# Kernel optimization log

Measured on AMD Instinct MI355X. Metric: run time of the kernel, lower is better.

The kernel has to match this reference:

```python
import jax, jax.numpy as jnp
import numpy as np

B, S, H, D = 8, 2048, 16, 64  # batch, seq, heads, head_dim
DM = H * D                    # d_model = 1024
W = 4                         # compression window / stride


def setup_inputs() -> dict:
    key = jax.random.key(0)
    ks = jax.random.split(key, 6)
    return {
        "pre_q": jax.random.normal(ks[0], (B, S, H, D), dtype=jnp.float32),
        "pre_k": jax.random.normal(ks[1], (B, S, H, D), dtype=jnp.float32),
        "pre_v": jax.random.normal(ks[2], (B, S, H, D), dtype=jnp.float32),
        "k_conv_kernel": jax.random.normal(ks[3], (W, D, D), dtype=jnp.float32) * (1.0 / np.sqrt(W * D)),
        "k_conv_bias": jnp.zeros((D,), dtype=jnp.float32),
        "v_conv_kernel": jax.random.normal(ks[4], (W, D, D), dtype=jnp.float32) * (1.0 / np.sqrt(W * D)),
        "v_conv_bias": jnp.zeros((D,), dtype=jnp.float32),
        "output_weights": jax.random.normal(ks[5], (DM, DM), dtype=jnp.float32) * (1.0 / np.sqrt(DM)),
        "compression_window": W,
    }


def _compress(x, kernel, bias, window):
    # x: [B, H, S, D] -> strided valid conv along seq -> [B, H, Sc, D]
    b, h, s, d = x.shape
    x2 = x.reshape(b * h, s, d)  # NWC
    y = jax.lax.conv_general_dilated(
        x2, kernel, window_strides=(window,), padding="VALID",
        dimension_numbers=("NWC", "WIO", "NWC")) + bias
    return y.reshape(b, h, -1, d)


def reference(pre_q, pre_k, pre_v, k_conv_kernel, k_conv_bias,
              v_conv_kernel, v_conv_bias, output_weights, compression_window):
    b, s, h, d = pre_q.shape
    q = jnp.transpose(pre_q, (0, 2, 1, 3))  # [B,H,S,D]
    k = jnp.transpose(pre_k, (0, 2, 1, 3))
    v = jnp.transpose(pre_v, (0, 2, 1, 3))
    kc = _compress(k, k_conv_kernel, k_conv_bias, compression_window)  # [B,H,Sc,D]
    vc = _compress(v, v_conv_kernel, v_conv_bias, compression_window)
    scale = 1.0 / np.sqrt(d).astype(np.float32)
    scores = jnp.einsum("bhsd,bhtd->bhst", q, kc) * scale  # [B,H,S,Sc]
    attn = jax.nn.softmax(scores, axis=-1)
    out = jnp.einsum("bhst,bhtd->bhsd", attn, vc)  # [B,H,S,D]
    out = jnp.transpose(out, (0, 2, 1, 3)).reshape(b, s, h * d)  # [B,S,DM]
    return out @ output_weights  # [B,S,DM]
```

## Files before the change

kernel.cpp:

```cpp
#include <hip/hip_runtime.h>
#include <hip/hip_bf16.h>
#include <math.h>

#define B_   8
#define S_   2048
#define H_   16
#define D_   64
#define DM_  1024
#define W_   4
#define SC_  512

typedef float f32x4 __attribute__((ext_vector_type(4)));
typedef short bf16x8 __attribute__((ext_vector_type(8)));
typedef short bf16x4 __attribute__((ext_vector_type(4)));

static __device__ inline short f2bf(float f) {
    union { float f; unsigned u; } v; v.f = f;
    unsigned r = v.u + 0x7fffu + ((v.u >> 16) & 1u);
    return (short)(r >> 16);
}

static __device__ inline short bfc(float f) {
    __hip_bfloat16 h = __float2bfloat16(f);
    union { __hip_bfloat16 h; short s; } u; u.h = h; return u.s;
}

static __device__ inline float fexp2(float x) {
    float r; asm("v_exp_f32 %0, %1" : "=v"(r) : "v"(x)); return r;
}

__global__ __launch_bounds__(256) void wtrans_kernel(
    const float* __restrict__ Wg, short* __restrict__ Wt)
{
    __shared__ float ws[64][68];
    const int tid = threadIdx.x;
    const int n0 = blockIdx.x * 64, k0 = blockIdx.y * 64;
    #pragma unroll
    for (int i = 0; i < 4; ++i) {
        int idx = i * 256 + tid;
        int row = idx >> 4, c4 = idx & 15;
        float4 v = *(const float4*)(Wg + (size_t)(k0 + row) * 1024 + n0 + c4 * 4);
        *(float4*)(&ws[row][c4 * 4]) = v;
    }
    __syncthreads();
    #pragma unroll
    for (int i = 0; i < 2; ++i) {
        int idx = i * 256 + tid;
        int n = idx >> 3, kc8 = idx & 7;
        bf16x8 o;
        #pragma unroll
        for (int j = 0; j < 8; ++j) o[j] = f2bf(ws[kc8 * 8 + j][n]);
        *(bf16x8*)(Wt + (size_t)(n0 + n) * 1024 + k0 + kc8 * 8) = o;
    }
}

__global__ __launch_bounds__(256) void prep_kernel(
    const float* __restrict__ kk, const float* __restrict__ vk,
    short* __restrict__ BkT)
{
    __shared__ float ws[64][68];
    const int tid = threadIdx.x;
    const int k0 = blockIdx.x * 64;
    const float* src = blockIdx.y ? vk : kk;
    short* dst = BkT + (size_t)blockIdx.y * 64 * 256;
    #pragma unroll
    for (int i = 0; i < 4; ++i) {
        int idx = i * 256 + tid;
        int row = idx >> 4, c4 = idx & 15;
        float4 v = *(const float4*)(src + (size_t)(k0 + row) * 64 + c4 * 4);
        *(float4*)(&ws[row][c4 * 4]) = v;
    }
    __syncthreads();
    #pragma unroll
    for (int i = 0; i < 2; ++i) {
        int idx = i * 256 + tid;
        int n = idx >> 3, kc8 = idx & 7;
        bf16x8 o;
        #pragma unroll
        for (int j = 0; j < 8; ++j) o[j] = f2bf(ws[kc8 * 8 + j][n]);
        *(bf16x8*)(dst + (size_t)n * 256 + k0 + kc8 * 8) = o;
    }
}

template<int TR>
__global__ __launch_bounds__(256) void compress_mfma(
    const float* __restrict__ x,
    const short* __restrict__ bkt,
    const float* __restrict__ bias,
    short* __restrict__ y)
{
    __shared__ __align__(16) char Ah[16384];
    __shared__ __align__(16) char Al[16384];
    __shared__ __align__(16) char Bs[32768];
    const int tid  = threadIdx.x;
    const int bid  = (blockIdx.x & 7) * 256 + (blockIdx.x >> 3);
    const int tile = bid & 15;
    const int bh   = bid >> 4;
    const int h    = bh & 15;
    const int b    = bh >> 4;
    const int t0   = tile * 32;
    const int s0   = t0 * 4;

    #pragma unroll
    for (int i = 0; i < 8; ++i) {
        int idx = i * 256 + tid;
        int sl = idx >> 4, c4 = idx & 15;
        float4 v = *(const float4*)(x + (((size_t)(b * S_ + s0 + sl) * H_ + h) * D_) + c4 * 4);
        int tl = sl >> 2, k = (sl & 3) * 64 + c4 * 4;
        bf16x4 h4, l4;
        #pragma unroll
        for (int j = 0; j < 4; ++j) {
            float f = ((const float*)&v)[j];
            short hs = f2bf(f);
            union { unsigned u; float f; } hf; hf.u = ((unsigned)(unsigned short)hs) << 16;
            h4[j] = hs;
            l4[j] = f2bf(f - hf.f);
        }
        int base = (tl * 256 + k) * 2;
        int sw = (tl & 7) << 4;
        *(bf16x4*)(Ah + (base ^ sw)) = h4;
        *(bf16x4*)(Al + (base ^ sw)) = l4;
    }
    #pragma unroll
    for (int i = 0; i < 8; ++i) {
        int idx = i * 256 + tid;
        int dr = idx >> 5, part = idx & 31;
        bf16x8 bv = *(const bf16x8*)(bkt + dr * 256 + part * 8);
        *(bf16x8*)(Bs + ((dr * 512 + part * 16) ^ ((dr & 7) << 4))) = bv;
    }

    const int w = tid >> 6, ln = tid & 63, ln15 = ln & 15, hi = ln >> 4;
    const int wm = w & 1, wn = w >> 1;
    f32x4 acc[2];
    #pragma unroll
    for (int nf = 0; nf < 2; ++nf) {
        float bv = bias[wn * 32 + nf * 16 + ln15];
        acc[nf] = (f32x4){bv, bv, bv, bv};
    }
    __syncthreads();

    const int arow = wm * 16 + ln15;
    const int asw  = (arow & 7) << 4;
    #pragma unroll
    for (int kst = 0; kst < 16; ++kst) {
        const char* Asel = (kst < 8) ? Ah : Al;
        int kb = (kst & 7) * 64 + hi * 16;
        bf16x8 af = *(const bf16x8*)(Asel + ((arow * 512 + kb) ^ asw));
        #pragma unroll
        for (int nf = 0; nf < 2; ++nf) {
            int br = wn * 32 + nf * 16 + ln15;
            bf16x8 b8 = *(const bf16x8*)(Bs + ((br * 512 + kb) ^ ((br & 7) << 4)));
            acc[nf] = __builtin_amdgcn_mfma_f32_16x16x32_bf16(af, b8, acc[nf], 0, 0, 0);
        }
    }

    #pragma unroll
    for (int nf = 0; nf < 2; ++nf) {
        int dout = wn * 32 + nf * 16 + ln15;
        #pragma unroll
        for (int r = 0; r < 4; ++r) {
            float vv = acc[nf][r];
            if (!TR) {
                int t = t0 + wm * 16 + hi * 4 + r;
                y[((size_t)bh * SC_ + t) * 64 + dout] = f2bf(vv);
            } else {
                int p = r + 4 * wm + 8 * hi;
                y[((size_t)bh * 64 + dout) * SC_ + t0 + p] = f2bf(vv);
            }
        }
    }
}

__global__ __launch_bounds__(1024) void attn_kernel(
    const float* __restrict__ q,
    const short* __restrict__ kc,
    const short* __restrict__ vct,
    short* __restrict__ xb)
{
    extern __shared__ __align__(16) char smem[];
    char* klds = smem;
    char* vlds = smem + 65536;

    const int tid  = threadIdx.x;
    const int bid  = (blockIdx.x & 7) * 128 + (blockIdx.x >> 3);
    const int qc   = bid & 7;
    const int bh   = bid >> 3;
    const int h    = bh & 15;
    const int b    = bh >> 4;
    const int w    = tid >> 6;
    const int ln   = tid & 63;
    const int ln15 = ln & 15;
    const int hi   = ln >> 4;
    const int sbase = qc * 256 + w * 16;
    const int swz  = (ln15 & 7) << 4;

    const short* kg = kc + (size_t)bh * SC_ * 64;
    const short* vg = vct + (size_t)bh * 64 * SC_;

    #pragma unroll
    for (int i = 0; i < 4; ++i) {
        int idx = i * 1024 + tid;
        int row = idx >> 3, part = idx & 7;
        bf16x8 kv = *(const bf16x8*)(kg + idx * 8);
        *(bf16x8*)(klds + ((row * 128 + part * 16) ^ ((row & 7) << 4))) = kv;
    }
    #pragma unroll
    for (int i = 0; i < 4; ++i) {
        int idx = i * 1024 + tid;
        int row = idx >> 6, part = idx & 63;
        bf16x8 vv = *(const bf16x8*)(vg + idx * 8);
        *(bf16x8*)(vlds + ((row * 1024 + part * 16) ^ ((row & 7) << 4))) = vv;
    }

    bf16x8 qb[2];
    {
        const float* qrow = q + (((size_t)(b * S_ + sbase + ln15)) * H_ + h) * D_;
        const float qs = 0.18033688011112042f;
        #pragma unroll
        for (int dblk = 0; dblk < 2; ++dblk) {
            const float* p = qrow + dblk * 32 + hi * 8;
            #pragma unroll
            for (int j = 0; j < 8; ++j) qb[dblk][j] = bfc(p[j] * qs);
        }
    }

    f32x4 oacc[4];
    #pragma unroll
    for (int ns = 0; ns < 4; ++ns) oacc[ns] = (f32x4){0.f, 0.f, 0.f, 0.f};
    float mrun = -1e30f, lrun = 0.f;

    __syncthreads();

    #pragma unroll 2
    for (int kt = 0; kt < 8; ++kt) {
        f32x4 dsc[4];
        __builtin_amdgcn_s_setprio(1);
        #pragma unroll
        for (int ks = 0; ks < 4; ++ks) {
            int rbase = (kt * 64 + ks * 16 + ln15) * 128;
            bf16x8 ka0 = *(const bf16x8*)(klds + ((rbase + hi * 16) ^ swz));
            bf16x8 ka1 = *(const bf16x8*)(klds + ((rbase + 64 + hi * 16) ^ swz));
            dsc[ks] = __builtin_amdgcn_mfma_f32_16x16x32_bf16(ka0, qb[0], (f32x4){0.f,0.f,0.f,0.f}, 0, 0, 0);
            dsc[ks] = __builtin_amdgcn_mfma_f32_16x16x32_bf16(ka1, qb[1], dsc[ks], 0, 0, 0);
        }
        __builtin_amdgcn_s_setprio(0);

        float tm = -1e30f;
        #pragma unroll
        for (int ks = 0; ks < 4; ++ks)
            #pragma unroll
            for (int r = 0; r < 4; ++r) tm = fmaxf(tm, dsc[ks][r]);
        tm = fmaxf(tm, __shfl_xor(tm, 16));
        tm = fmaxf(tm, __shfl_xor(tm, 32));

        if (!__all(tm <= mrun + 11.0f)) {
            float mn = fmaxf(mrun, tm);
            float f = fexp2(mrun - mn);
            mrun = mn;
            lrun *= f;
            float fr[4];
            #pragma unroll
            for (int r = 0; r < 4; ++r) fr[r] = __shfl(f, hi * 4 + r);
            #pragma unroll
            for (int ns = 0; ns < 4; ++ns)
                #pragma unroll
                for (int r = 0; r < 4; ++r) oacc[ns][r] *= fr[r];
        }

        bf16x8 pa[2];
        float lp = 0.f;
        #pragma unroll
        for (int ks = 0; ks < 4; ++ks)
            #pragma unroll
            for (int r = 0; r < 4; ++r) {
                float e = fexp2(dsc[ks][r] - mrun);
                lp += e;
                pa[ks >> 1][(ks & 1) * 4 + r] = bfc(e);
            }
        lp += __shfl_xor(lp, 16);
        lp += __shfl_xor(lp, 32);
        lrun += lp;

        __builtin_amdgcn_s_setprio(1);
        #pragma unroll
        for (int kb = 0; kb < 2; ++kb)
            #pragma unroll
            for (int ns = 0; ns < 4; ++ns) {
                int rbase = (ns * 16 + ln15) * 1024;
                bf16x8 vb = *(const bf16x8*)(vlds + ((rbase + kt * 128 + kb * 64 + hi * 16) ^ swz));
                oacc[ns] = __builtin_amdgcn_mfma_f32_16x16x32_bf16(pa[kb], vb, oacc[ns], 0, 0, 0);
            }
        __builtin_amdgcn_s_setprio(0);
    }

    float li[4];
    #pragma unroll
    for (int r = 0; r < 4; ++r) li[r] = 1.f / __shfl(lrun, hi * 4 + r);
    #pragma unroll
    for (int ns = 0; ns < 4; ++ns)
        #pragma unroll
        for (int r = 0; r < 4; ++r) {
            size_t idx = ((size_t)(b * S_ + sbase + hi * 4 + r)) * DM_ + h * 64 + ns * 16 + ln15;
            xb[idx] = f2bf(oacc[ns][r] * li[r]);
        }
}

__global__ __launch_bounds__(256) void proj_kernel(
    const short* __restrict__ Xb,
    const short* __restrict__ Wt,
    float* __restrict__ out)
{
    __shared__ __align__(16) char As[8192];
    __shared__ __align__(16) char Bs[8192];
    const int tid  = threadIdx.x;
    const int wid  = tid >> 6;
    const int ln   = tid & 63;
    const int ln15 = ln & 15;
    const int hi   = ln >> 4;
    const int wr   = wid >> 1, wc = wid & 1;
    const int m0   = blockIdx.y * 128, n0 = blockIdx.x * 128;
    const int srow = tid >> 2, spart = tid & 3;

    f32x4 acc[4][4];
    #pragma unroll
    for (int i = 0; i < 4; ++i)
        #pragma unroll
        for (int j = 0; j < 4; ++j) acc[i][j] = (f32x4){0.f, 0.f, 0.f, 0.f};

    bf16x8 a0 = *(const bf16x8*)(Xb + (size_t)(m0 + srow) * 1024 + spart * 8);
    bf16x8 a1 = *(const bf16x8*)(Xb + (size_t)(m0 + srow + 64) * 1024 + spart * 8);
    bf16x8 b0 = *(const bf16x8*)(Wt + (size_t)(n0 + srow) * 1024 + spart * 8);
    bf16x8 b1 = *(const bf16x8*)(Wt + (size_t)(n0 + srow + 64) * 1024 + spart * 8);

    for (int k0 = 0; k0 < 1024; k0 += 32) {
        __syncthreads();
        *(bf16x8*)(As + ((srow * 64 + spart * 16) ^ ((srow & 7) << 4))) = a0;
        *(bf16x8*)(As + (((srow + 64) * 64 + spart * 16) ^ (((srow + 64) & 7) << 4))) = a1;
        *(bf16x8*)(Bs + ((srow * 64 + spart * 16) ^ ((srow & 7) << 4))) = b0;
        *(bf16x8*)(Bs + (((srow + 64) * 64 + spart * 16) ^ (((srow + 64) & 7) << 4))) = b1;
        __syncthreads();
        if (k0 < 992) {
            a0 = *(const bf16x8*)(Xb + (size_t)(m0 + srow) * 1024 + k0 + 32 + spart * 8);
            a1 = *(const bf16x8*)(Xb + (size_t)(m0 + srow + 64) * 1024 + k0 + 32 + spart * 8);
            b0 = *(const bf16x8*)(Wt + (size_t)(n0 + srow) * 1024 + k0 + 32 + spart * 8);
            b1 = *(const bf16x8*)(Wt + (size_t)(n0 + srow + 64) * 1024 + k0 + 32 + spart * 8);
        }
        bf16x8 af[4], bfr[4];
        #pragma unroll
        for (int mf = 0; mf < 4; ++mf) {
            int row = wr * 64 + mf * 16 + ln15;
            af[mf] = *(const bf16x8*)(As + ((row * 64 + hi * 16) ^ ((row & 7) << 4)));
        }
        #pragma unroll
        for (int nf = 0; nf < 4; ++nf) {
            int row = wc * 64 + nf * 16 + ln15;
            bfr[nf] = *(const bf16x8*)(Bs + ((row * 64 + hi * 16) ^ ((row & 7) << 4)));
        }
        #pragma unroll
        for (int mf = 0; mf < 4; ++mf)
            #pragma unroll
            for (int nf = 0; nf < 4; ++nf)
                acc[mf][nf] = __builtin_amdgcn_mfma_f32_16x16x32_bf16(af[mf], bfr[nf], acc[mf][nf], 0, 0, 0);
    }

    #pragma unroll
    for (int mf = 0; mf < 4; ++mf)
        #pragma unroll
        for (int nf = 0; nf < 4; ++nf)
            #pragma unroll
            for (int r = 0; r < 4; ++r)
                out[(size_t)(m0 + wr * 64 + mf * 16 + hi * 4 + r) * 1024 + n0 + wc * 64 + nf * 16 + ln15] =
                    acc[mf][nf][r];
}

extern "C" void kernel_launch(void* const* d_in, const int* in_sizes, int n_in,
                              void* d_out, int out_size, void* d_ws, size_t ws_size,
                              hipStream_t stream) {
    const float* pre_q = (const float*)d_in[0];
    const float* pre_k = (const float*)d_in[1];
    const float* pre_v = (const float*)d_in[2];
    const float* kkern = (const float*)d_in[3];
    const float* kbias = (const float*)d_in[4];
    const float* vkern = (const float*)d_in[5];
    const float* vbias = (const float*)d_in[6];
    const float* wout  = (const float*)d_in[7];
    float* out = (float*)d_out;

    short* Xb  = (short*)d_ws;
    short* kcb = Xb + (size_t)(B_ * S_) * DM_;
    short* vct = kcb + (size_t)B_ * H_ * SC_ * D_;
    short* Wtb = vct + (size_t)B_ * H_ * SC_ * D_;
    short* BkT = Wtb + (size_t)DM_ * DM_;

    prep_kernel<<<dim3(4, 2), 256, 0, stream>>>(kkern, vkern, BkT);
    wtrans_kernel<<<dim3(16, 16), 256, 0, stream>>>(wout, Wtb);
    compress_mfma<0><<<B_ * H_ * 16, 256, 0, stream>>>(pre_k, BkT, kbias, kcb);
    compress_mfma<1><<<B_ * H_ * 16, 256, 0, stream>>>(pre_v, BkT + 64 * 256, vbias, vct);
    attn_kernel<<<B_ * H_ * (S_ / 256), 1024, 131072, stream>>>(pre_q, kcb, vct, Xb);
    proj_kernel<<<dim3(DM_ / 128, (B_ * S_) / 128), 256, 0, stream>>>(Xb, Wtb, out);
}
```

Before: 181.8 us.

## Process two query fragments per wave in attention and use direct-to-LDS loads in projection

The attention kernel now has each wave handle 32 query rows as two 16-row fragments. Each K and V fragment read from LDS feeds twice as many MFMAs, and the grid is halved, so each K/V tile is staged into LDS half as often. The projection GEMM drops register-staged LDS stores in favour of global_load_lds with a 64-wide K step, and remaps block indices for better L2 locality. In exchange, register pressure roughly doubles in attention. Projection loses its register prefetch overlap and its LDS swizzle, which risks LDS bank conflicts.

```diff
diff --git a/kernel.cpp b/kernel.cpp
--- a/kernel.cpp
+++ b/kernel.cpp
@@ -27,6 +27,12 @@
 
 static __device__ inline float fexp2(float x) {
     float r; asm("v_exp_f32 %0, %1" : "=v"(r) : "v"(x)); return r;
+}
+
+static __device__ inline void gll16(const void* g, void* l) {
+    __builtin_amdgcn_global_load_lds(
+        (const __attribute__((address_space(1))) unsigned int*)g,
+        (__attribute__((address_space(3))) unsigned int*)l, 16, 0, 0);
 }
 
 __global__ __launch_bounds__(256) void wtrans_kernel(
@@ -182,16 +188,16 @@
     char* vlds = smem + 65536;
 
     const int tid  = threadIdx.x;
-    const int bid  = (blockIdx.x & 7) * 128 + (blockIdx.x >> 3);
-    const int qc   = bid & 7;
-    const int bh   = bid >> 3;
+    const int bid  = (blockIdx.x & 7) * 64 + (blockIdx.x >> 3);
+    const int qc   = bid & 3;
+    const int bh   = bid >> 2;
     const int h    = bh & 15;
     const int b    = bh >> 4;
     const int w    = tid >> 6;
     const int ln   = tid & 63;
     const int ln15 = ln & 15;
     const int hi   = ln >> 4;
-    const int sbase = qc * 256 + w * 16;
+    const int sbase = qc * 512 + w * 32;
     const int swz  = (ln15 & 7) << 4;
 
     const short* kg = kc + (size_t)bh * SC_ * 64;
@@ -212,96 +218,138 @@
         *(bf16x8*)(vlds + ((row * 1024 + part * 16) ^ ((row & 7) << 4))) = vv;
     }
 
-    bf16x8 qb[2];
+    bf16x8 qb[2][2];
     {
-        const float* qrow = q + (((size_t)(b * S_ + sbase + ln15)) * H_ + h) * D_;
         const float qs = 0.18033688011112042f;
         #pragma unroll
-        for (int dblk = 0; dblk < 2; ++dblk) {
-            const float* p = qrow + dblk * 32 + hi * 8;
-            #pragma unroll
-            for (int j = 0; j < 8; ++j) qb[dblk][j] = bfc(p[j] * qs);
-        }
-    }
-
-    f32x4 oacc[4];
-    #pragma unroll
-    for (int ns = 0; ns < 4; ++ns) oacc[ns] = (f32x4){0.f, 0.f, 0.f, 0.f};
-    float mrun = -1e30f, lrun = 0.f;
+        for (int qf = 0; qf < 2; ++qf) {
+            const float* qrow = q + (((size_t)(b * S_ + sbase + qf * 16 + ln15)) * H_ + h) * D_;
+            #pragma unroll
+            for (int dblk = 0; dblk < 2; ++dblk) {
+                const float* p = qrow + dblk * 32 + hi * 8;
+                #pragma unroll
+                for (int j = 0; j < 8; ++j) qb[qf][dblk][j] = bfc(p[j] * qs);
+            }
+        }
+    }
+
+    const char* kp0 = klds + ln15 * 128 + ((hi * 16) ^ swz);
+    const char* kp1 = klds + ln15 * 128 + ((64 + hi * 16) ^ swz);
+    const char* vp0 = vlds + ln15 * 1024 + ((hi * 16) ^ swz);
+    const char* vp1 = vlds + ln15 * 1024 + ((64 + hi * 16) ^ swz);
+
+    f32x4 oa0[4], oa1[4];
+    #pragma unroll
+    for (int ns = 0; ns < 4; ++ns) {
+        oa0[ns] = (f32x4){0.f, 0.f, 0.f, 0.f};
+        oa1[ns] = (f32x4){0.f, 0.f, 0.f, 0.f};
+    }
+    float mrun0 = -1e30f, lrun0 = 0.f;
+    float mrun1 = -1e30f, lrun1 = 0.f;
 
     __syncthreads();
 
-    #pragma unroll 2
+    #pragma unroll
     for (int kt = 0; kt < 8; ++kt) {
-        f32x4 dsc[4];
+        f32x4 d0[4], d1[4];
         __builtin_amdgcn_s_setprio(1);
         #pragma unroll
         for (int ks = 0; ks < 4; ++ks) {
-            int rbase = (kt * 64 + ks * 16 + ln15) * 128;
-            bf16x8 ka0 = *(const bf16x8*)(klds + ((rbase + hi * 16) ^ swz));
-            bf16x8 ka1 = *(const bf16x8*)(klds + ((rbase + 64 + hi * 16) ^ swz));
-            dsc[ks] = __builtin_amdgcn_mfma_f32_16x16x32_bf16(ka0, qb[0], (f32x4){0.f,0.f,0.f,0.f}, 0, 0, 0);
-            dsc[ks] = __builtin_amdgcn_mfma_f32_16x16x32_bf16(ka1, qb[1], dsc[ks], 0, 0, 0);
+            bf16x8 ka0 = *(const bf16x8*)(kp0 + kt * 8192 + ks * 2048);
+            bf16x8 ka1 = *(const bf16x8*)(kp1 + kt * 8192 + ks * 2048);
+            d0[ks] = __builtin_amdgcn_mfma_f32_16x16x32_bf16(ka0, qb[0][0], (f32x4){0.f,0.f,0.f,0.f}, 0, 0, 0);
+            d0[ks] = __builtin_amdgcn_mfma_f32_16x16x32_bf16(ka1, qb[0][1], d0[ks], 0, 0, 0);
+            d1[ks] = __builtin_amdgcn_mfma_f32_16x16x32_bf16(ka0, qb[1][0], (f32x4){0.f,0.f,0.f,0.f}, 0, 0, 0);
+            d1[ks] = __builtin_amdgcn_mfma_f32_16x16x32_bf16(ka1, qb[1][1], d1[ks], 0, 0, 0);
         }
         __builtin_amdgcn_s_setprio(0);
 
-        float tm = -1e30f;
+        float tm0 = -1e30f, tm1 = -1e30f;
         #pragma unroll
         for (int ks = 0; ks < 4; ++ks)
             #pragma unroll
-            for (int r = 0; r < 4; ++r) tm = fmaxf(tm, dsc[ks][r]);
-        tm = fmaxf(tm, __shfl_xor(tm, 16));
-        tm = fmaxf(tm, __shfl_xor(tm, 32));
-
-        if (!__all(tm <= mrun + 11.0f)) {
-            float mn = fmaxf(mrun, tm);
-            float f = fexp2(mrun - mn);
-            mrun = mn;
-            lrun *= f;
+            for (int r = 0; r < 4; ++r) {
+                tm0 = fmaxf(tm0, d0[ks][r]);
+                tm1 = fmaxf(tm1, d1[ks][r]);
+            }
+        tm0 = fmaxf(tm0, __shfl_xor(tm0, 16));
+        tm0 = fmaxf(tm0, __shfl_xor(tm0, 32));
+        tm1 = fmaxf(tm1, __shfl_xor(tm1, 16));
+        tm1 = fmaxf(tm1, __shfl_xor(tm1, 32));
+
+        if (!__all(tm0 <= mrun0 + 11.0f)) {
+            float mn = fmaxf(mrun0, tm0);
+            float f = fexp2(mrun0 - mn);
+            mrun0 = mn;
+            lrun0 *= f;
             float fr[4];
             #pragma unroll
             for (int r = 0; r < 4; ++r) fr[r] = __shfl(f, hi * 4 + r);
             #pragma unroll
             for (int ns = 0; ns < 4; ++ns)
                 #pragma unroll
-                for (int r = 0; r < 4; ++r) oacc[ns][r] *= fr[r];
-        }
-
-        bf16x8 pa[2];
-        float lp = 0.f;
+                for (int r = 0; r < 4; ++r) oa0[ns][r] *= fr[r];
+        }
+        if (!__all(tm1 <= mrun1 + 11.0f)) {
+            float mn = fmaxf(mrun1, tm1);
+            float f = fexp2(mrun1 - mn);
+            mrun1 = mn;
+            lrun1 *= f;
+            float fr[4];
+            #pragma unroll
+            for (int r = 0; r < 4; ++r) fr[r] = __shfl(f, hi * 4 + r);
+            #pragma unroll
+            for (int ns = 0; ns < 4; ++ns)
+                #pragma unroll
+                for (int r = 0; r < 4; ++r) oa1[ns][r] *= fr[r];
+        }
+
+        bf16x8 pa0[2], pa1[2];
+        float lp0 = 0.f, lp1 = 0.f;
         #pragma unroll
         for (int ks = 0; ks < 4; ++ks)
             #pragma unroll
             for (int r = 0; r < 4; ++r) {
-                float e = fexp2(dsc[ks][r] - mrun);
-                lp += e;
-                pa[ks >> 1][(ks & 1) * 4 + r] = bfc(e);
+                float e0 = fexp2(d0[ks][r] - mrun0);
+                float e1 = fexp2(d1[ks][r] - mrun1);
+                lp0 += e0; lp1 += e1;
+                pa0[ks >> 1][(ks & 1) * 4 + r] = bfc(e0);
+                pa1[ks >> 1][(ks & 1) * 4 + r] = bfc(e1);
             }
-        lp += __shfl_xor(lp, 16);
-        lp += __shfl_xor(lp, 32);
-        lrun += lp;
+        lp0 += __shfl_xor(lp0, 16);
+        lp0 += __shfl_xor(lp0, 32);
+        lp1 += __shfl_xor(lp1, 16);
+        lp1 += __shfl_xor(lp1, 32);
+        lrun0 += lp0;
+        lrun1 += lp1;
 
         __builtin_amdgcn_s_setprio(1);
         #pragma unroll
-        for (int kb = 0; kb < 2; ++kb)
-            #pragma unroll
-            for (int ns = 0; ns < 4; ++ns) {
-                int rbase = (ns * 16 + ln15) * 1024;
-                bf16x8 vb = *(const bf16x8*)(vlds + ((rbase + kt * 128 + kb * 64 + hi * 16) ^ swz));
-                oacc[ns] = __builtin_amdgcn_mfma_f32_16x16x32_bf16(pa[kb], vb, oacc[ns], 0, 0, 0);
-            }
+        for (int ns = 0; ns < 4; ++ns) {
+            bf16x8 vb0 = *(const bf16x8*)(vp0 + ns * 16384 + kt * 128);
+            bf16x8 vb1 = *(const bf16x8*)(vp1 + ns * 16384 + kt * 128);
+            oa0[ns] = __builtin_amdgcn_mfma_f32_16x16x32_bf16(pa0[0], vb0, oa0[ns], 0, 0, 0);
+            oa0[ns] = __builtin_amdgcn_mfma_f32_16x16x32_bf16(pa0[1], vb1, oa0[ns], 0, 0, 0);
+            oa1[ns] = __builtin_amdgcn_mfma_f32_16x16x32_bf16(pa1[0], vb0, oa1[ns], 0, 0, 0);
+            oa1[ns] = __builtin_amdgcn_mfma_f32_16x16x32_bf16(pa1[1], vb1, oa1[ns], 0, 0, 0);
+        }
         __builtin_amdgcn_s_setprio(0);
     }
 
-    float li[4];
-    #pragma unroll
-    for (int r = 0; r < 4; ++r) li[r] = 1.f / __shfl(lrun, hi * 4 + r);
+    float li0[4], li1[4];
+    #pragma unroll
+    for (int r = 0; r < 4; ++r) {
+        li0[r] = 1.f / __shfl(lrun0, hi * 4 + r);
+        li1[r] = 1.f / __shfl(lrun1, hi * 4 + r);
+    }
     #pragma unroll
     for (int ns = 0; ns < 4; ++ns)
         #pragma unroll
         for (int r = 0; r < 4; ++r) {
-            size_t idx = ((size_t)(b * S_ + sbase + hi * 4 + r)) * DM_ + h * 64 + ns * 16 + ln15;
-            xb[idx] = f2bf(oacc[ns][r] * li[r]);
+            size_t i0 = ((size_t)(b * S_ + sbase + hi * 4 + r)) * DM_ + h * 64 + ns * 16 + ln15;
+            xb[i0] = f2bf(oa0[ns][r] * li0[r]);
+            size_t i1 = ((size_t)(b * S_ + sbase + 16 + hi * 4 + r)) * DM_ + h * 64 + ns * 16 + ln15;
+            xb[i1] = f2bf(oa1[ns][r] * li1[r]);
         }
 }
 
@@ -310,16 +358,18 @@
     const short* __restrict__ Wt,
     float* __restrict__ out)
 {
-    __shared__ __align__(16) char As[8192];
-    __shared__ __align__(16) char Bs[8192];
+    __shared__ __align__(16) short As[128 * 64];
+    __shared__ __align__(16) short Bs[128 * 64];
     const int tid  = threadIdx.x;
     const int wid  = tid >> 6;
     const int ln   = tid & 63;
     const int ln15 = ln & 15;
     const int hi   = ln >> 4;
     const int wr   = wid >> 1, wc = wid & 1;
-    const int m0   = blockIdx.y * 128, n0 = blockIdx.x * 128;
-    const int srow = tid >> 2, spart = tid & 3;
+    const int bid  = (blockIdx.x & 7) * 128 + (blockIdx.x >> 3);
+    const int tn   = bid & 7, tm = bid >> 3;
+    const int m0   = tm * 128, n0 = tn * 128;
+    const int spart = tid & 7;
 
     f32x4 acc[4][4];
     #pragma unroll
@@ -327,40 +377,32 @@
         #pragma unroll
         for (int j = 0; j < 4; ++j) acc[i][j] = (f32x4){0.f, 0.f, 0.f, 0.f};
 
-    bf16x8 a0 = *(const bf16x8*)(Xb + (size_t)(m0 + srow) * 1024 + spart * 8);
-    bf16x8 a1 = *(const bf16x8*)(Xb + (size_t)(m0 + srow + 64) * 1024 + spart * 8);
-    bf16x8 b0 = *(const bf16x8*)(Wt + (size_t)(n0 + srow) * 1024 + spart * 8);
-    bf16x8 b1 = *(const bf16x8*)(Wt + (size_t)(n0 + srow + 64) * 1024 + spart * 8);
-
-    for (int k0 = 0; k0 < 1024; k0 += 32) {
+    for (int k0 = 0; k0 < 1024; k0 += 64) {
+        #pragma unroll
+        for (int i = 0; i < 4; ++i) {
+            int row = (i * 256 + tid) >> 3;
+            int ldsoff = __builtin_amdgcn_readfirstlane((i * 256 + (tid & ~63)) * 16);
+            gll16(Xb + (size_t)(m0 + row) * 1024 + k0 + spart * 8, (char*)As + ldsoff);
+            gll16(Wt + (size_t)(n0 + row) * 1024 + k0 + spart * 8, (char*)Bs + ldsoff);
+        }
         __syncthreads();
-        *(bf16x8*)(As + ((srow * 64 + spart * 16) ^ ((srow & 7) << 4))) = a0;
-        *(bf16x8*)(As + (((srow + 64) * 64 + spart * 16) ^ (((srow + 64) & 7) << 4))) = a1;
-        *(bf16x8*)(Bs + ((srow * 64 + spart * 16) ^ ((srow & 7) << 4))) = b0;
-        *(bf16x8*)(Bs + (((srow + 64) * 64 + spart * 16) ^ (((srow + 64) & 7) << 4))) = b1;
+
+        #pragma unroll
+        for (int ks = 0; ks < 2; ++ks) {
+            bf16x8 af[4], bfr[4];
+            #pragma unroll
+            for (int mf = 0; mf < 4; ++mf)
+                af[mf] = *(const bf16x8*)((const char*)As + (wr * 64 + mf * 16 + ln15) * 128 + ks * 64 + hi * 16);
+            #pragma unroll
+            for (int nf = 0; nf < 4; ++nf)
+                bfr[nf] = *(const bf16x8*)((const char*)Bs + (wc * 64 + nf * 16 + ln15) * 128 + ks * 64 + hi * 16);
+            #pragma unroll
+            for (int mf = 0; mf < 4; ++mf)
+                #pragma unroll
+                for (int nf = 0; nf < 4; ++nf)
+                    acc[mf][nf] = __builtin_amdgcn_mfma_f32_16x16x32_bf16(af[mf], bfr[nf], acc[mf][nf], 0, 0, 0);
+        }
         __syncthreads();
-        if (k0 < 992) {
-            a0 = *(const bf16x8*)(Xb + (size_t)(m0 + srow) * 1024 + k0 + 32 + spart * 8);
-            a1 = *(const bf16x8*)(Xb + (size_t)(m0 + srow + 64) * 1024 + k0 + 32 + spart * 8);
-            b0 = *(const bf16x8*)(Wt + (size_t)(n0 + srow) * 1024 + k0 + 32 + spart * 8);
-            b1 = *(const bf16x8*)(Wt + (size_t)(n0 + srow + 64) * 1024 + k0 + 32 + spart * 8);
-        }
-        bf16x8 af[4], bfr[4];
-        #pragma unroll
-        for (int mf = 0; mf < 4; ++mf) {
-            int row = wr * 64 + mf * 16 + ln15;
-            af[mf] = *(const bf16x8*)(As + ((row * 64 + hi * 16) ^ ((row & 7) << 4)));
-        }
-        #pragma unroll
-        for (int nf = 0; nf < 4; ++nf) {
-            int row = wc * 64 + nf * 16 + ln15;
-            bfr[nf] = *(const bf16x8*)(Bs + ((row * 64 + hi * 16) ^ ((row & 7) << 4)));
-        }
-        #pragma unroll
-        for (int mf = 0; mf < 4; ++mf)
-            #pragma unroll
-            for (int nf = 0; nf < 4; ++nf)
-                acc[mf][nf] = __builtin_amdgcn_mfma_f32_16x16x32_bf16(af[mf], bfr[nf], acc[mf][nf], 0, 0, 0);
     }
 
     #pragma unroll
@@ -396,6 +438,6 @@
     wtrans_kernel<<<dim3(16, 16), 256, 0, stream>>>(wout, Wtb);
     compress_mfma<0><<<B_ * H_ * 16, 256, 0, stream>>>(pre_k, BkT, kbias, kcb);
     compress_mfma<1><<<B_ * H_ * 16, 256, 0, stream>>>(pre_v, BkT + 64 * 256, vbias, vct);
-    attn_kernel<<<B_ * H_ * (S_ / 256), 1024, 131072, stream>>>(pre_q, kcb, vct, Xb);
-    proj_kernel<<<dim3(DM_ / 128, (B_ * S_) / 128), 256, 0, stream>>>(Xb, Wtb, out);
-}
+    attn_kernel<<<B_ * H_ * (S_ / 512), 1024, 131072, stream>>>(pre_q, kcb, vct, Xb);
+    proj_kernel<<<DM_ / 128 * ((B_ * S_) / 128), 256, 0, stream>>>(Xb, Wtb, out);
+}
```

New measurement: 169.9 us. -6.5%, faster.
